# Kernel tuning notes

Measured on AMD Instinct MI355X. Metric: run time of the kernel, lower is better.

The kernel has to match this reference:

```python
import jax, jax.numpy as jnp
import numpy as np

N, E, IN, HID, H, OUT = 50000, 1600000, 64, 128, 4, 64
D = HID // H  # per-head dim = 32
EPS = 1e-5
NEG_SLOPE = 0.2


def layer_norm(x, g, b):
    mu = x.mean(-1, keepdims=True)
    var = ((x - mu) ** 2).mean(-1, keepdims=True)
    return (x - mu) * jax.lax.rsqrt(var + EPS) * g + b


def gat_conv(h, src, dst, W, a_src, a_dst, bias):
    # h: [N, HID]; W: [HID, H*D]; a_src/a_dst: [H, D]
    hW = (h @ W).reshape(N, H, D)
    e_src = (hW * a_src).sum(-1)  # [N, H]
    e_dst = (hW * a_dst).sum(-1)  # [N, H]
    e = jax.nn.leaky_relu(e_src[src] + e_dst[dst], NEG_SLOPE)  # [Etot, H]
    m = jax.ops.segment_max(e, dst, num_segments=N)            # [N, H]
    ex = jnp.exp(e - m[dst])
    denom = jax.ops.segment_sum(ex, dst, num_segments=N)       # [N, H]
    alpha = ex / denom[dst]                                    # [Etot, H]
    out = jax.ops.segment_sum(alpha[:, :, None] * hW[src], dst, num_segments=N)
    return out.reshape(N, H * D) + bias


def setup_inputs():
    key = jax.random.key(0)
    ks = jax.random.split(key, 16)
    s = 0.05
    return {
        "x": jax.random.normal(ks[0], (N, IN), jnp.float32),
        "edge_index": jax.random.randint(ks[1], (2, E), 0, N, jnp.int64),
        "w_in": jax.random.normal(ks[2], (IN, HID), jnp.float32) * s,
        "b_in": jnp.zeros((HID,), jnp.float32),
        "g1": jnp.ones((HID,), jnp.float32),
        "be1": jnp.zeros((HID,), jnp.float32),
        "W1": jax.random.normal(ks[3], (HID, H * D), jnp.float32) * s,
        "as1": jax.random.normal(ks[4], (H, D), jnp.float32) * s,
        "ad1": jax.random.normal(ks[5], (H, D), jnp.float32) * s,
        "bg1": jnp.zeros((H * D,), jnp.float32),
        "g2": jnp.ones((HID,), jnp.float32),
        "be2": jnp.zeros((HID,), jnp.float32),
        "W2": jax.random.normal(ks[6], (HID, H * D), jnp.float32) * s,
        "as2": jax.random.normal(ks[7], (H, D), jnp.float32) * s,
        "ad2": jax.random.normal(ks[8], (H, D), jnp.float32) * s,
        "bg2": jnp.zeros((H * D,), jnp.float32),
        "w_out": jax.random.normal(ks[9], (HID, OUT), jnp.float32) * s,
        "b_out": jnp.zeros((OUT,), jnp.float32),
    }


def reference(x, edge_index, w_in, b_in, g1, be1, W1, as1, ad1, bg1,
              g2, be2, W2, as2, ad2, bg2, w_out, b_out):
    # PyG GATConv default add_self_loops=True
    loops = jnp.arange(N, dtype=edge_index.dtype)
    src = jnp.concatenate([edge_index[0], loops])
    dst = jnp.concatenate([edge_index[1], loops])

    h = x @ w_in + b_in
    h = jax.nn.gelu(layer_norm(h, g1, be1))
    h = gat_conv(h, src, dst, W1, as1, ad1, bg1)
    h = jax.nn.gelu(layer_norm(h, g2, be2))
    # dropout: identity in eval mode
    h = gat_conv(h, src, dst, W2, as2, ad2, bg2)
    return h @ w_out + b_out
```

## Files before the change

### kernel.cpp

```cpp
#include <hip/hip_runtime.h>
#include <hip/hip_bf16.h>
#include <math.h>

#define NN   50000
#define EE   1600000
#define ETOT (EE + NN)
#define HID  128
#define INF_ 64
#define OUTF 64

#define NBK  1024
#define NPB  49
#define CAP  3072
#define BBLK 256
#define CHUNK ((ETOT + BBLK - 1) / BBLK)

#define PADX 72
#define PADH 136

typedef short  short8  __attribute__((ext_vector_type(8)));
typedef float  floatx4 __attribute__((ext_vector_type(4)));
typedef float  floatx2 __attribute__((ext_vector_type(2)));

__device__ __forceinline__ ushort f2b(float f) {
    __hip_bfloat16 h = __float2bfloat16(f);
    return *reinterpret_cast<ushort*>(&h);
}

__device__ __forceinline__ float gelu_f(float x) {
    float x2 = x * x;
    float u  = 0.7978845608f * fmaf(0.044715f * x2, x, x);
    u = fminf(u, 40.f);
    float t = __expf(2.f * u);
    return x * t / (t + 1.f);
}


__global__ __launch_bounds__(1024) void k_bucket(const int* __restrict__ ei,
                                                 int* bcur, int* __restrict__ tmp) {
    __shared__ unsigned sortedv[CHUNK];
    __shared__ int hist[NBK], gbase[NBK], loff[NBK], lcur[NBK];
    int t = threadIdx.x;
    int lo = blockIdx.x * CHUNK;
    int hi = min(lo + CHUNK, ETOT);
    int bsize = hi - lo;
    hist[t] = 0;
    __syncthreads();
    for (int i = lo + t; i < hi; i += 1024) {
        int d = (i < EE) ? ei[EE + i] : i - EE;
        atomicAdd(&hist[d / NPB], 1);
    }
    __syncthreads();
    {
        int c = hist[t];
        gbase[t] = (c > 0) ? atomicAdd(&bcur[t], c) : 0;
        loff[t] = c;
    }
    __syncthreads();
    for (int d = 1; d < NBK; d <<= 1) {
        int v = (t >= d) ? loff[t - d] : 0;
        __syncthreads();
        loff[t] += v;
        __syncthreads();
    }
    {
        int ex = loff[t] - hist[t];
        __syncthreads();
        loff[t] = ex;
        lcur[t] = ex;
    }
    __syncthreads();
    for (int i = lo + t; i < hi; i += 1024) {
        unsigned s, d;
        if (i < EE) { s = (unsigned)ei[i]; d = (unsigned)ei[EE + i]; }
        else        { s = d = (unsigned)(i - EE); }
        unsigned b = d / NPB;
        int p = atomicAdd(&lcur[b], 1);
        sortedv[p] = (b << 22) | (s << 6) | (d - b * NPB);
    }
    __syncthreads();
    for (int i = t; i < bsize; i += 1024) {
        unsigned v = sortedv[i];
        unsigned b = v >> 22;
        int pp = gbase[b] + i - loff[b];
        if (pp < CAP) tmp[b * CAP + pp] = (int)(v & 0x3FFFFFu);
    }
}

__global__ __launch_bounds__(1024) void k_bscan(const int* __restrict__ bcur,
                                                int* __restrict__ bstart,
                                                int* __restrict__ off,
                                                int* __restrict__ csr) {
    __shared__ int s[NBK];
    int t = threadIdx.x;
    int v0 = bcur[t];
    s[t] = v0;
    __syncthreads();
    for (int d = 1; d < NBK; d <<= 1) {
        int v = (t >= d) ? s[t - d] : 0;
        __syncthreads();
        s[t] += v;
        __syncthreads();
    }
    bstart[t] = s[t] - v0;
    if (t == 0) off[NN] = ETOT;
    if (t < 64) csr[ETOT + t] = 0;
}

__global__ __launch_bounds__(256) void k_bucket2csr(const int* __restrict__ tmp,
                                                    const int* __restrict__ bcur,
                                                    const int* __restrict__ bstart,
                                                    int* __restrict__ off,
                                                    int* __restrict__ csr,
                                                    int* __restrict__ dstid) {
    __shared__ int sE[CAP];
    __shared__ int lcnt[NPB];
    __shared__ int loff[NPB];
    int b = blockIdx.x, t = threadIdx.x;
    int n0    = b * NPB;
    int bsize = min(bcur[b], CAP);
    int base  = bstart[b];
    if (t < NPB) lcnt[t] = 0;
    for (int i = t; i < bsize; i += 256) sE[i] = tmp[b * CAP + i];
    __syncthreads();
    for (int i = t; i < bsize; i += 256) atomicAdd(&lcnt[sE[i] & 63], 1);
    __syncthreads();
    if (t == 0) {
        int run = 0;
        for (int j = 0; j < NPB; ++j) { loff[j] = run; run += lcnt[j]; }
    }
    __syncthreads();
    if (t < NPB) {
        if (n0 + t < NN) off[n0 + t] = base + loff[t];
        lcnt[t] = loff[t];
    }
    __syncthreads();
    for (int i = t; i < bsize; i += 256) {
        int v   = sE[i];
        int d   = v & 63;
        int pos = base + atomicAdd(&lcnt[d], 1);
        csr[pos]   = v >> 6;
        dstid[pos] = n0 + d;
    }
}


__global__ void k_packall(const float* __restrict__ w_in, const float* __restrict__ W1,
                          const float* __restrict__ W2, ushort* __restrict__ Bp1,
                          ushort* __restrict__ BpW1, ushort* __restrict__ BpW2,
                          int* __restrict__ bcur) {
    int tid = blockIdx.x * 256 + threadIdx.x;
    if (tid < NBK) bcur[tid] = 0;
    const float* W; ushort* dst; int K, id;
    if (tid < 1024)      { W = w_in; dst = Bp1;  K = 64;  id = tid; }
    else if (tid < 3072) { W = W1;   dst = BpW1; K = 128; id = tid - 1024; }
    else if (tid < 5120) { W = W2;   dst = BpW2; K = 128; id = tid - 3072; }
    else return;
    int kst = K >> 5;
    int l = id & 63;
    int s = (id >> 6) % kst;
    int T = id / (kst * 64);
    int m = l & 15, q = l >> 4;
    ushort o[8];
    #pragma unroll
    for (int j = 0; j < 8; ++j)
        o[j] = f2b(W[(s * 32 + q * 8 + j) * 128 + T * 16 + m]);
    uint4 pk;
    pk.x = (unsigned)o[0] | ((unsigned)o[1] << 16);
    pk.y = (unsigned)o[2] | ((unsigned)o[3] << 16);
    pk.z = (unsigned)o[4] | ((unsigned)o[5] << 16);
    pk.w = (unsigned)o[6] | ((unsigned)o[7] << 16);
    reinterpret_cast<uint4*>(dst)[id] = pk;
}

__device__ __forceinline__ void pack_store_fp8(ushort* hbfw, int l, int n0w, bool active,
                                               uint* __restrict__ hW8) {
    if (!active) return;
    int row = l >> 2, ch = l & 3;
    uint ov[8];
    #pragma unroll
    for (int u = 0; u < 8; ++u) {
        int c0 = ch * 32 + u * 4;
        float f0 = __uint_as_float((uint)hbfw[row * PADH + c0 + 0] << 16);
        float f1 = __uint_as_float((uint)hbfw[row * PADH + c0 + 1] << 16);
        float f2 = __uint_as_float((uint)hbfw[row * PADH + c0 + 2] << 16);
        float f3 = __uint_as_float((uint)hbfw[row * PADH + c0 + 3] << 16);
        int pk = __builtin_amdgcn_cvt_pk_fp8_f32(f0, f1, 0, false);
        pk     = __builtin_amdgcn_cvt_pk_fp8_f32(f2, f3, pk, true);
        ov[u] = (uint)pk;
    }
    uint4* dst = reinterpret_cast<uint4*>(hW8 + (size_t)(n0w + row) * 32 + ch * 8);
    dst[0] = make_uint4(ov[0], ov[1], ov[2], ov[3]);
    dst[1] = make_uint4(ov[4], ov[5], ov[6], ov[7]);
}


__global__ __launch_bounds__(128) void k_infeat(const float* __restrict__ x,
                                                const ushort* __restrict__ Bp1,
                                                const float* __restrict__ bin,
                                                const float* __restrict__ g,
                                                const float* __restrict__ be,
                                                const ushort* __restrict__ Bp2,
                                                const float* __restrict__ asrc,
                                                const float* __restrict__ adst,
                                                uint* __restrict__ hW8,
                                                float* __restrict__ esrc,
                                                float* __restrict__ edst) {
    __shared__ ushort xbf[2][16 * PADX];
    __shared__ ushort hbf[2][16 * PADH];
    int t = threadIdx.x, w = t >> 6, l = t & 63;
    int m = l & 15, q = l >> 4;
    int n0w = blockIdx.x * 32 + w * 16;
    bool active = (n0w < NN);
    int nb = active ? n0w : 0;

    const float4* x4 = reinterpret_cast<const float4*>(x) + (size_t)nb * 16;
    #pragma unroll
    for (int i = 0; i < 4; ++i) {
        int f4 = l + 64 * i;
        int node = f4 >> 4, c4 = f4 & 15;
        float4 v = x4[f4];
        ushort4 pk = { f2b(v.x), f2b(v.y), f2b(v.z), f2b(v.w) };
        *reinterpret_cast<ushort4*>(&xbf[w][node * PADX + c4 * 4]) = pk;
    }
    __syncthreads();

    const short8* B1 = reinterpret_cast<const short8*>(Bp1);
    floatx4 acc1[8];
    #pragma unroll
    for (int T = 0; T < 8; ++T) acc1[T] = (floatx4){0.f, 0.f, 0.f, 0.f};
    #pragma unroll
    for (int s = 0; s < 2; ++s) {
        short8 a = *reinterpret_cast<const short8*>(&xbf[w][m * PADX + s * 32 + q * 8]);
        #pragma unroll
        for (int T = 0; T < 8; ++T) {
            short8 b = B1[(T * 2 + s) * 64 + l];
            acc1[T] = __builtin_amdgcn_mfma_f32_16x16x32_bf16(a, b, acc1[T], 0, 0, 0);
        }
    }

    float bc[8], gc[8], bec[8];
    #pragma unroll
    for (int T = 0; T < 8; ++T) {
        int c = T * 16 + m;
        bc[T] = bin[c]; gc[T] = g[c]; bec[T] = be[c];
    }
    #pragma unroll
    for (int j = 0; j < 4; ++j) {
        float s1 = 0.f, s2 = 0.f;
        #pragma unroll
        for (int T = 0; T < 8; ++T) {
            float v = acc1[T][j] + bc[T];
            s1 += v; s2 = fmaf(v, v, s2);
        }
        #pragma unroll
        for (int mk = 1; mk < 16; mk <<= 1) {
            s1 += __shfl_xor(s1, mk, 64);
            s2 += __shfl_xor(s2, mk, 64);
        }
        float mu = s1 * (1.f / 128.f);
        float var = s2 * (1.f / 128.f) - mu * mu;
        float rs = rsqrtf(var + 1e-5f);
        #pragma unroll
        for (int T = 0; T < 8; ++T) {
            float v = acc1[T][j] + bc[T];
            float y = (v - mu) * rs * gc[T] + bec[T];
            hbf[w][(q * 4 + j) * PADH + T * 16 + m] = f2b(gelu_f(y));
        }
    }
    __syncthreads();

    const short8* B2 = reinterpret_cast<const short8*>(Bp2);
    floatx4 acc2[8];
    #pragma unroll
    for (int T = 0; T < 8; ++T) acc2[T] = (floatx4){0.f, 0.f, 0.f, 0.f};
    #pragma unroll
    for (int s = 0; s < 4; ++s) {
        short8 a = *reinterpret_cast<const short8*>(&hbf[w][m * PADH + s * 32 + q * 8]);
        #pragma unroll
        for (int T = 0; T < 8; ++T) {
            short8 b = B2[(T * 4 + s) * 64 + l];
            acc2[T] = __builtin_amdgcn_mfma_f32_16x16x32_bf16(a, b, acc2[T], 0, 0, 0);
        }
    }

    __syncthreads();
    #pragma unroll
    for (int j = 0; j < 4; ++j)
        #pragma unroll
        for (int T = 0; T < 8; ++T)
            hbf[w][(q * 4 + j) * PADH + T * 16 + m] = f2b(acc2[T][j]);
    __syncthreads();
    pack_store_fp8(hbf[w], l, n0w, active, hW8);

    float as_[8], ad_[8];
    #pragma unroll
    for (int T = 0; T < 8; ++T) {
        int c = T * 16 + m;
        as_[T] = asrc[c]; ad_[T] = adst[c];
    }
    #pragma unroll
    for (int j = 0; j < 4; ++j) {
        #pragma unroll
        for (int h = 0; h < 4; ++h) {
            float v1 = fmaf(acc2[2 * h][j], as_[2 * h], acc2[2 * h + 1][j] * as_[2 * h + 1]);
            float v2 = fmaf(acc2[2 * h][j], ad_[2 * h], acc2[2 * h + 1][j] * ad_[2 * h + 1]);
            #pragma unroll
            for (int mk = 1; mk < 16; mk <<= 1) {
                v1 += __shfl_xor(v1, mk, 64);
                v2 += __shfl_xor(v2, mk, 64);
            }
            if (m == 0 && active) {
                esrc[(n0w + q * 4 + j) * 4 + h] = v1;
                edst[(n0w + q * 4 + j) * 4 + h] = v2;
            }
        }
    }
}


__global__ __launch_bounds__(128) void k_feat(const float* __restrict__ hin,
                                              const float* __restrict__ g,
                                              const float* __restrict__ be,
                                              const ushort* __restrict__ Bp2,
                                              const float* __restrict__ asrc,
                                              const float* __restrict__ adst,
                                              uint* __restrict__ hW8,
                                              float* __restrict__ esrc,
                                              float* __restrict__ edst) {
    __shared__ ushort hbf[2][16 * PADH];
    int t = threadIdx.x, w = t >> 6, l = t & 63;
    int m = l & 15, q = l >> 4;
    int n0w = blockIdx.x * 32 + w * 16;
    bool active = (n0w < NN);
    int nb = active ? n0w : 0;

    const float4* h4g = reinterpret_cast<const float4*>(hin) + (size_t)nb * 32;
    const float4* g4  = reinterpret_cast<const float4*>(g);
    const float4* be4 = reinterpret_cast<const float4*>(be);
    #pragma unroll
    for (int i = 0; i < 8; ++i) {
        int f4 = l + 64 * i;
        int node = f4 >> 5, c4 = f4 & 31;
        float4 v = h4g[f4];
        float s1 = v.x + v.y + v.z + v.w;
        float s2 = fmaf(v.x, v.x, fmaf(v.y, v.y, fmaf(v.z, v.z, v.w * v.w)));
        #pragma unroll
        for (int mk = 1; mk < 32; mk <<= 1) {
            s1 += __shfl_xor(s1, mk, 64);
            s2 += __shfl_xor(s2, mk, 64);
        }
        float mu = s1 * (1.f / 128.f);
        float var = s2 * (1.f / 128.f) - mu * mu;
        float rs = rsqrtf(var + 1e-5f);
        float4 gg = g4[c4], bb = be4[c4];
        ushort4 pk;
        pk.x = f2b(gelu_f((v.x - mu) * rs * gg.x + bb.x));
        pk.y = f2b(gelu_f((v.y - mu) * rs * gg.y + bb.y));
        pk.z = f2b(gelu_f((v.z - mu) * rs * gg.z + bb.z));
        pk.w = f2b(gelu_f((v.w - mu) * rs * gg.w + bb.w));
        *reinterpret_cast<ushort4*>(&hbf[w][node * PADH + c4 * 4]) = pk;
    }
    __syncthreads();

    const short8* B2 = reinterpret_cast<const short8*>(Bp2);
    floatx4 acc2[8];
    #pragma unroll
    for (int T = 0; T < 8; ++T) acc2[T] = (floatx4){0.f, 0.f, 0.f, 0.f};
    #pragma unroll
    for (int s = 0; s < 4; ++s) {
        short8 a = *reinterpret_cast<const short8*>(&hbf[w][m * PADH + s * 32 + q * 8]);
        #pragma unroll
        for (int T = 0; T < 8; ++T) {
            short8 b = B2[(T * 4 + s) * 64 + l];
            acc2[T] = __builtin_amdgcn_mfma_f32_16x16x32_bf16(a, b, acc2[T], 0, 0, 0);
        }
    }

    __syncthreads();
    #pragma unroll
    for (int j = 0; j < 4; ++j)
        #pragma unroll
        for (int T = 0; T < 8; ++T)
            hbf[w][(q * 4 + j) * PADH + T * 16 + m] = f2b(acc2[T][j]);
    __syncthreads();
    pack_store_fp8(hbf[w], l, n0w, active, hW8);

    float as_[8], ad_[8];
    #pragma unroll
    for (int T = 0; T < 8; ++T) {
        int c = T * 16 + m;
        as_[T] = asrc[c]; ad_[T] = adst[c];
    }
    #pragma unroll
    for (int j = 0; j < 4; ++j) {
        #pragma unroll
        for (int h = 0; h < 4; ++h) {
            float v1 = fmaf(acc2[2 * h][j], as_[2 * h], acc2[2 * h + 1][j] * as_[2 * h + 1]);
            float v2 = fmaf(acc2[2 * h][j], ad_[2 * h], acc2[2 * h + 1][j] * ad_[2 * h + 1]);
            #pragma unroll
            for (int mk = 1; mk < 16; mk <<= 1) {
                v1 += __shfl_xor(v1, mk, 64);
                v2 += __shfl_xor(v2, mk, 64);
            }
            if (m == 0 && active) {
                esrc[(n0w + q * 4 + j) * 4 + h] = v1;
                edst[(n0w + q * 4 + j) * 4 + h] = v2;
            }
        }
    }
}


__global__ __launch_bounds__(256) void k_edgew(const int* __restrict__ csr,
                                               const int* __restrict__ dstid,
                                               const float* __restrict__ esrc,
                                               const float* __restrict__ edst,
                                               ushort* __restrict__ wexp) {
    int i = blockIdx.x * 256 + threadIdx.x;
    if (i >= ETOT) return;
    int s = csr[i], d = dstid[i];
    float4 es = reinterpret_cast<const float4*>(esrc)[s];
    float4 ed = reinterpret_cast<const float4*>(edst)[d];
    float e0 = es.x + ed.x, e1 = es.y + ed.y, e2 = es.z + ed.z, e3 = es.w + ed.w;
    e0 = __expf(fmaxf(e0, 0.2f * e0));
    e1 = __expf(fmaxf(e1, 0.2f * e1));
    e2 = __expf(fmaxf(e2, 0.2f * e2));
    e3 = __expf(fmaxf(e3, 0.2f * e3));
    ushort4 pk = { f2b(e0), f2b(e1), f2b(e2), f2b(e3) };
    reinterpret_cast<ushort4*>(wexp)[i] = pk;
}


__global__ __launch_bounds__(128) void k_gat(const uint* __restrict__ hW8,
                                             const ushort* __restrict__ wexp,
                                             const int* __restrict__ off,
                                             const int* __restrict__ csr,
                                             const float* __restrict__ bg,
                                             float* __restrict__ out) {
    __shared__ float redA[16][8];
    __shared__ float redD[16];
    int n = blockIdx.x, t = threadIdx.x;
    int wv = t >> 6, l = t & 63;
    int slot = l >> 4;
    int q    = l & 15;
    int hq   = q >> 2;
    int o0 = off[n], o1 = off[n + 1];
    const uint2* hw2 = reinterpret_cast<const uint2*>(hW8);
    floatx2 a01 = {0.f, 0.f}, a23 = {0.f, 0.f}, a45 = {0.f, 0.f}, a67 = {0.f, 0.f};
    float dsum = 0.f;
    int nIter = (o1 - o0 + 15) >> 4;
    int e = o0 + wv * 4 + slot;

    int    srcA = csr[e];      ushort ubA = wexp[e * 4 + hq];
    int    srcB = csr[e + 8];  ushort ubB = wexp[(e + 8) * 4 + hq];
    int    srcC = csr[e + 16]; ushort ubC = wexp[(e + 16) * 4 + hq];
    int    srcD = csr[e + 24]; ushort ubD = wexp[(e + 24) * 4 + hq];
    uint2  rA = hw2[(size_t)srcA * 16 + q];
    uint2  rB = hw2[(size_t)srcB * 16 + q];

    for (int it = 0; it < nIter; ++it) {
        uint2 rC = hw2[(size_t)srcC * 16 + q];
        uint2 rD = hw2[(size_t)srcD * 16 + q];
        int    srcE = csr[e + 32]; ushort ubE = wexp[(e + 32) * 4 + hq];
        int    srcF = csr[e + 40]; ushort ubF = wexp[(e + 40) * 4 + hq];
        float wa = (e     < o1) ? __uint_as_float(((unsigned)ubA) << 16) : 0.f;
        float wb = (e + 8 < o1) ? __uint_as_float(((unsigned)ubB) << 16) : 0.f;
        floatx2 wa2 = {wa, wa}, wb2 = {wb, wb};
        a01 += wa2 * __builtin_amdgcn_cvt_pk_f32_fp8(rA.x, false);
        a23 += wa2 * __builtin_amdgcn_cvt_pk_f32_fp8(rA.x, true);
        a45 += wa2 * __builtin_amdgcn_cvt_pk_f32_fp8(rA.y, false);
        a67 += wa2 * __builtin_amdgcn_cvt_pk_f32_fp8(rA.y, true);
        a01 += wb2 * __builtin_amdgcn_cvt_pk_f32_fp8(rB.x, false);
        a23 += wb2 * __builtin_amdgcn_cvt_pk_f32_fp8(rB.x, true);
        a45 += wb2 * __builtin_amdgcn_cvt_pk_f32_fp8(rB.y, false);
        a67 += wb2 * __builtin_amdgcn_cvt_pk_f32_fp8(rB.y, true);
        dsum += wa + wb;
        e += 16;
        rA = rC; rB = rD;
        srcC = srcE; srcD = srcF;
        ubA = ubC; ubB = ubD; ubC = ubE; ubD = ubF;
    }
    float acc[8] = {a01[0], a01[1], a23[0], a23[1], a45[0], a45[1], a67[0], a67[1]};
    #pragma unroll
    for (int mk = 16; mk <= 32; mk <<= 1) {
        #pragma unroll
        for (int j = 0; j < 8; ++j) acc[j] += __shfl_xor(acc[j], mk, 64);
        dsum += __shfl_xor(dsum, mk, 64);
    }
    if (wv == 1 && l < 16) {
        #pragma unroll
        for (int j = 0; j < 8; ++j) redA[l][j] = acc[j];
        redD[l] = dsum;
    }
    __syncthreads();
    if (wv == 0 && l < 16) {
        float inv = 1.0f / (dsum + redD[l]);
        float4 r0, r1;
        r0.x = (acc[0] + redA[l][0]) * inv + bg[l * 8 + 0];
        r0.y = (acc[1] + redA[l][1]) * inv + bg[l * 8 + 1];
        r0.z = (acc[2] + redA[l][2]) * inv + bg[l * 8 + 2];
        r0.w = (acc[3] + redA[l][3]) * inv + bg[l * 8 + 3];
        r1.x = (acc[4] + redA[l][4]) * inv + bg[l * 8 + 4];
        r1.y = (acc[5] + redA[l][5]) * inv + bg[l * 8 + 5];
        r1.z = (acc[6] + redA[l][6]) * inv + bg[l * 8 + 6];
        r1.w = (acc[7] + redA[l][7]) * inv + bg[l * 8 + 7];
        float4* op = reinterpret_cast<float4*>(out + (size_t)n * HID + l * 8);
        op[0] = r0; op[1] = r1;
    }
}


__global__ __launch_bounds__(64) void k_out(const float* __restrict__ h,
                                            const float* __restrict__ w,
                                            const float* __restrict__ b,
                                            float* __restrict__ out) {
    __shared__ __align__(16) float hr[16 * 132];
    int t = threadIdx.x, n0 = blockIdx.x * 16;
    const float4* h4g = reinterpret_cast<const float4*>(h) + (size_t)n0 * 32;
    float4* hr4 = reinterpret_cast<float4*>(hr);
    #pragma unroll
    for (int i = 0; i < 8; ++i) {
        int f4 = t + 64 * i;
        hr4[(f4 >> 5) * 33 + (f4 & 31)] = h4g[f4];
    }
    __syncthreads();
    int cg = t & 15, ng = t >> 4;
    const float4* w4 = reinterpret_cast<const float4*>(w);
    float4 bb = reinterpret_cast<const float4*>(b)[cg];
    float4 acc[4] = {bb, bb, bb, bb};
    for (int k4 = 0; k4 < 32; ++k4) {
        float4 w0 = w4[(k4 * 4 + 0) * 16 + cg];
        float4 w1 = w4[(k4 * 4 + 1) * 16 + cg];
        float4 w2 = w4[(k4 * 4 + 2) * 16 + cg];
        float4 w3 = w4[(k4 * 4 + 3) * 16 + cg];
        #pragma unroll
        for (int r = 0; r < 4; ++r) {
            float4 hv = hr4[(ng * 4 + r) * 33 + k4];
            acc[r].x = fmaf(hv.x, w0.x, fmaf(hv.y, w1.x, fmaf(hv.z, w2.x, fmaf(hv.w, w3.x, acc[r].x))));
            acc[r].y = fmaf(hv.x, w0.y, fmaf(hv.y, w1.y, fmaf(hv.z, w2.y, fmaf(hv.w, w3.y, acc[r].y))));
            acc[r].z = fmaf(hv.x, w0.z, fmaf(hv.y, w1.z, fmaf(hv.z, w2.z, fmaf(hv.w, w3.z, acc[r].z))));
            acc[r].w = fmaf(hv.x, w0.w, fmaf(hv.y, w1.w, fmaf(hv.z, w2.w, fmaf(hv.w, w3.w, acc[r].w))));
        }
    }
    float4* o4 = reinterpret_cast<float4*>(out) + (size_t)n0 * 16;
    #pragma unroll
    for (int r = 0; r < 4; ++r) o4[(ng * 4 + r) * 16 + cg] = acc[r];
}

extern "C" void kernel_launch(void* const* d_in, const int* in_sizes, int n_in,
                              void* d_out, int out_size, void* d_ws, size_t ws_size,
                              hipStream_t stream) {
    const float* x    = (const float*)d_in[0];
    const int*   ei   = (const int*)  d_in[1];
    const float* w_in = (const float*)d_in[2];
    const float* b_in = (const float*)d_in[3];
    const float* g1   = (const float*)d_in[4];
    const float* be1  = (const float*)d_in[5];
    const float* W1   = (const float*)d_in[6];
    const float* as1  = (const float*)d_in[7];
    const float* ad1  = (const float*)d_in[8];
    const float* bg1  = (const float*)d_in[9];
    const float* g2   = (const float*)d_in[10];
    const float* be2  = (const float*)d_in[11];
    const float* W2   = (const float*)d_in[12];
    const float* as2  = (const float*)d_in[13];
    const float* ad2  = (const float*)d_in[14];
    const float* bg2  = (const float*)d_in[15];
    const float* w_o  = (const float*)d_in[16];
    const float* b_o  = (const float*)d_in[17];
    float* out = (float*)d_out;

    char* p = (char*)d_ws;
    auto take = [&](size_t bytes) {
        void* r = p;
        p += (bytes + 255) & ~(size_t)255;
        return r;
    };
    float*  gout  = (float*)take((size_t)NN * HID * 4);
    float*  h2    = (float*)take((size_t)NN * HID * 4);
    uint*   hW8   = (uint*)take((size_t)NN * HID);
    float*  esrc  = (float*)take((size_t)NN * 4 * 4);
    float*  edst  = (float*)take((size_t)NN * 4 * 4);
    int*    off   = (int*)take((size_t)(NN + 1) * 4);
    int*    csr   = (int*)take((size_t)(ETOT + 64) * 4);
    int*    dstid = (int*)take((size_t)ETOT * 4);
    size_t ovl = (size_t)ETOT * 8 + 512;
    size_t tsz = (size_t)NBK * CAP * 4;
    ushort* wexp  = (ushort*)take(ovl > tsz ? ovl : tsz);
    int*    tmp   = (int*)wexp;
    int*    bcur  = (int*)take((size_t)NBK * 4);
    int*    bstart= (int*)take((size_t)NBK * 4);
    ushort* Bp1   = (ushort*)take((size_t)1024 * 16);
    ushort* BpW1  = (ushort*)take((size_t)2048 * 16);
    ushort* BpW2  = (ushort*)take((size_t)2048 * 16);

    k_packall   <<<20, 256, 0, stream>>>(w_in, W1, W2, Bp1, BpW1, BpW2, bcur);
    k_bucket    <<<BBLK, 1024, 0, stream>>>(ei, bcur, tmp);
    k_bscan     <<<1, NBK, 0, stream>>>(bcur, bstart, off, csr);
    k_bucket2csr<<<NBK, 256, 0, stream>>>(tmp, bcur, bstart, off, csr, dstid);

    int gfeat = (NN + 31) / 32;
    k_infeat<<<gfeat, 128, 0, stream>>>(x, Bp1, b_in, g1, be1, BpW1, as1, ad1, hW8, esrc, edst);
    k_edgew <<<(ETOT + 255) / 256, 256, 0, stream>>>(csr, dstid, esrc, edst, wexp);
    k_gat   <<<NN, 128, 0, stream>>>(hW8, wexp, off, csr, bg1, gout);
    k_feat  <<<gfeat, 128, 0, stream>>>(gout, g2, be2, BpW2, as2, ad2, hW8, esrc, edst);
    k_edgew <<<(ETOT + 255) / 256, 256, 0, stream>>>(csr, dstid, esrc, edst, wexp);
    k_gat   <<<NN, 128, 0, stream>>>(hW8, wexp, off, csr, bg2, h2);
    k_out   <<<NN / 16, 64, 0, stream>>>(h2, w_o, b_o, out);
}
```

Baseline: 304.4 us.

## Fuse edge attention weights into GAT aggregation and drop dstid/wexp buffers

Removes the separate k_edgew pass, so the aggregation kernel now computes the leaky-relu and exp of esrc[src]+edst[dst] inline from per-node scores. This eliminates the dstid array and the bf16 wexp buffer along with their global writes and reads. The CSR build now uses 256 buckets of 196 nodes with a larger capacity, and k_bucket2csr uses 512 threads and a parallel scan. k_out processes 32 nodes per block with a bounds guard. The trade-off is a dependent gather of esrc per edge plus an exp per edge inside k_gat, and a larger per-bucket shared memory footprint in the CSR build.

```diff
diff --git a/kernel.cpp b/kernel.cpp
--- a/kernel.cpp
+++ b/kernel.cpp
@@ -9,9 +9,9 @@
 #define INF_ 64
 #define OUTF 64
 
-#define NBK  1024
-#define NPB  49
-#define CAP  3072
+#define NBK  256
+#define NPB  196
+#define CAP  8192
 #define BBLK 256
 #define CHUNK ((ETOT + BBLK - 1) / BBLK)
 
@@ -44,28 +44,27 @@
     int lo = blockIdx.x * CHUNK;
     int hi = min(lo + CHUNK, ETOT);
     int bsize = hi - lo;
-    hist[t] = 0;
+    if (t < NBK) hist[t] = 0;
     __syncthreads();
     for (int i = lo + t; i < hi; i += 1024) {
         int d = (i < EE) ? ei[EE + i] : i - EE;
         atomicAdd(&hist[d / NPB], 1);
     }
     __syncthreads();
-    {
+    if (t < NBK) {
         int c = hist[t];
         gbase[t] = (c > 0) ? atomicAdd(&bcur[t], c) : 0;
         loff[t] = c;
     }
     __syncthreads();
     for (int d = 1; d < NBK; d <<= 1) {
-        int v = (t >= d) ? loff[t - d] : 0;
+        int v = (t >= d && t < NBK) ? loff[t - d] : 0;
         __syncthreads();
-        loff[t] += v;
+        if (t < NBK) loff[t] += v;
         __syncthreads();
     }
-    {
+    if (t < NBK) {
         int ex = loff[t] - hist[t];
-        __syncthreads();
         loff[t] = ex;
         lcur[t] = ex;
     }
@@ -76,21 +75,21 @@
         else        { s = d = (unsigned)(i - EE); }
         unsigned b = d / NPB;
         int p = atomicAdd(&lcur[b], 1);
-        sortedv[p] = (b << 22) | (s << 6) | (d - b * NPB);
+        sortedv[p] = (b << 24) | (s << 8) | (d - b * NPB);
     }
     __syncthreads();
     for (int i = t; i < bsize; i += 1024) {
         unsigned v = sortedv[i];
-        unsigned b = v >> 22;
+        unsigned b = v >> 24;
         int pp = gbase[b] + i - loff[b];
-        if (pp < CAP) tmp[b * CAP + pp] = (int)(v & 0x3FFFFFu);
-    }
-}
-
-__global__ __launch_bounds__(1024) void k_bscan(const int* __restrict__ bcur,
-                                                int* __restrict__ bstart,
-                                                int* __restrict__ off,
-                                                int* __restrict__ csr) {
+        if (pp < CAP) tmp[b * CAP + pp] = (int)(v & 0xFFFFFFu);
+    }
+}
+
+__global__ __launch_bounds__(256) void k_bscan(const int* __restrict__ bcur,
+                                               int* __restrict__ bstart,
+                                               int* __restrict__ off,
+                                               int* __restrict__ csr) {
     __shared__ int s[NBK];
     int t = threadIdx.x;
     int v0 = bcur[t];
@@ -107,12 +106,11 @@
     if (t < 64) csr[ETOT + t] = 0;
 }
 
-__global__ __launch_bounds__(256) void k_bucket2csr(const int* __restrict__ tmp,
+__global__ __launch_bounds__(512) void k_bucket2csr(const int* __restrict__ tmp,
                                                     const int* __restrict__ bcur,
                                                     const int* __restrict__ bstart,
                                                     int* __restrict__ off,
-                                                    int* __restrict__ csr,
-                                                    int* __restrict__ dstid) {
+                                                    int* __restrict__ csr) {
     __shared__ int sE[CAP];
     __shared__ int lcnt[NPB];
     __shared__ int loff[NPB];
@@ -121,26 +119,28 @@
     int bsize = min(bcur[b], CAP);
     int base  = bstart[b];
     if (t < NPB) lcnt[t] = 0;
-    for (int i = t; i < bsize; i += 256) sE[i] = tmp[b * CAP + i];
-    __syncthreads();
-    for (int i = t; i < bsize; i += 256) atomicAdd(&lcnt[sE[i] & 63], 1);
-    __syncthreads();
-    if (t == 0) {
-        int run = 0;
-        for (int j = 0; j < NPB; ++j) { loff[j] = run; run += lcnt[j]; }
-    }
-    __syncthreads();
+    for (int i = t; i < bsize; i += 512) sE[i] = tmp[b * CAP + i];
+    __syncthreads();
+    for (int i = t; i < bsize; i += 512) atomicAdd(&lcnt[sE[i] & 255], 1);
+    __syncthreads();
+    if (t < NPB) loff[t] = lcnt[t];
+    __syncthreads();
+    for (int d = 1; d < NPB; d <<= 1) {
+        int v = (t >= d && t < NPB) ? loff[t - d] : 0;
+        __syncthreads();
+        if (t < NPB) loff[t] += v;
+        __syncthreads();
+    }
     if (t < NPB) {
-        if (n0 + t < NN) off[n0 + t] = base + loff[t];
-        lcnt[t] = loff[t];
-    }
-    __syncthreads();
-    for (int i = t; i < bsize; i += 256) {
+        int ex = loff[t] - lcnt[t];
+        if (n0 + t < NN) off[n0 + t] = base + ex;
+        lcnt[t] = ex;
+    }
+    __syncthreads();
+    for (int i = t; i < bsize; i += 512) {
         int v   = sE[i];
-        int d   = v & 63;
-        int pos = base + atomicAdd(&lcnt[d], 1);
-        csr[pos]   = v >> 6;
-        dstid[pos] = n0 + d;
+        int pos = base + atomicAdd(&lcnt[v & 255], 1);
+        csr[pos] = v >> 8;
     }
 }
 
@@ -172,6 +172,7 @@
     pk.w = (unsigned)o[6] | ((unsigned)o[7] << 16);
     reinterpret_cast<uint4*>(dst)[id] = pk;
 }
+
 
 __device__ __forceinline__ void pack_store_fp8(ushort* hbfw, int l, int n0w, bool active,
                                                uint* __restrict__ hW8) {
@@ -412,28 +413,9 @@
 }
 
 
-__global__ __launch_bounds__(256) void k_edgew(const int* __restrict__ csr,
-                                               const int* __restrict__ dstid,
-                                               const float* __restrict__ esrc,
-                                               const float* __restrict__ edst,
-                                               ushort* __restrict__ wexp) {
-    int i = blockIdx.x * 256 + threadIdx.x;
-    if (i >= ETOT) return;
-    int s = csr[i], d = dstid[i];
-    float4 es = reinterpret_cast<const float4*>(esrc)[s];
-    float4 ed = reinterpret_cast<const float4*>(edst)[d];
-    float e0 = es.x + ed.x, e1 = es.y + ed.y, e2 = es.z + ed.z, e3 = es.w + ed.w;
-    e0 = __expf(fmaxf(e0, 0.2f * e0));
-    e1 = __expf(fmaxf(e1, 0.2f * e1));
-    e2 = __expf(fmaxf(e2, 0.2f * e2));
-    e3 = __expf(fmaxf(e3, 0.2f * e3));
-    ushort4 pk = { f2b(e0), f2b(e1), f2b(e2), f2b(e3) };
-    reinterpret_cast<ushort4*>(wexp)[i] = pk;
-}
-
-
 __global__ __launch_bounds__(128) void k_gat(const uint* __restrict__ hW8,
-                                             const ushort* __restrict__ wexp,
+                                             const float* __restrict__ esrc,
+                                             const float* __restrict__ edst,
                                              const int* __restrict__ off,
                                              const int* __restrict__ csr,
                                              const float* __restrict__ bg,
@@ -446,26 +428,33 @@
     int q    = l & 15;
     int hq   = q >> 2;
     int o0 = off[n], o1 = off[n + 1];
+    float ednh = edst[n * 4 + hq];
     const uint2* hw2 = reinterpret_cast<const uint2*>(hW8);
     floatx2 a01 = {0.f, 0.f}, a23 = {0.f, 0.f}, a45 = {0.f, 0.f}, a67 = {0.f, 0.f};
     float dsum = 0.f;
     int nIter = (o1 - o0 + 15) >> 4;
     int e = o0 + wv * 4 + slot;
 
-    int    srcA = csr[e];      ushort ubA = wexp[e * 4 + hq];
-    int    srcB = csr[e + 8];  ushort ubB = wexp[(e + 8) * 4 + hq];
-    int    srcC = csr[e + 16]; ushort ubC = wexp[(e + 16) * 4 + hq];
-    int    srcD = csr[e + 24]; ushort ubD = wexp[(e + 24) * 4 + hq];
-    uint2  rA = hw2[(size_t)srcA * 16 + q];
-    uint2  rB = hw2[(size_t)srcB * 16 + q];
+    int srcA = csr[e];
+    int srcB = csr[e + 8];
+    int srcC = csr[e + 16];
+    int srcD = csr[e + 24];
+    float esA = esrc[srcA * 4 + hq];
+    float esB = esrc[srcB * 4 + hq];
+    uint2 rA = hw2[(size_t)srcA * 16 + q];
+    uint2 rB = hw2[(size_t)srcB * 16 + q];
 
     for (int it = 0; it < nIter; ++it) {
         uint2 rC = hw2[(size_t)srcC * 16 + q];
         uint2 rD = hw2[(size_t)srcD * 16 + q];
-        int    srcE = csr[e + 32]; ushort ubE = wexp[(e + 32) * 4 + hq];
-        int    srcF = csr[e + 40]; ushort ubF = wexp[(e + 40) * 4 + hq];
-        float wa = (e     < o1) ? __uint_as_float(((unsigned)ubA) << 16) : 0.f;
-        float wb = (e + 8 < o1) ? __uint_as_float(((unsigned)ubB) << 16) : 0.f;
+        float esC = esrc[srcC * 4 + hq];
+        float esD = esrc[srcD * 4 + hq];
+        int srcE = csr[e + 32];
+        int srcF = csr[e + 40];
+        float ea = esA + ednh; ea = fmaxf(ea, 0.2f * ea);
+        float eb = esB + ednh; eb = fmaxf(eb, 0.2f * eb);
+        float wa = (e     < o1) ? __expf(ea) : 0.f;
+        float wb = (e + 8 < o1) ? __expf(eb) : 0.f;
         floatx2 wa2 = {wa, wa}, wb2 = {wb, wb};
         a01 += wa2 * __builtin_amdgcn_cvt_pk_f32_fp8(rA.x, false);
         a23 += wa2 * __builtin_amdgcn_cvt_pk_f32_fp8(rA.x, true);
@@ -478,8 +467,8 @@
         dsum += wa + wb;
         e += 16;
         rA = rC; rB = rD;
+        esA = esC; esB = esD;
         srcC = srcE; srcD = srcF;
-        ubA = ubC; ubB = ubD; ubC = ubE; ubD = ubF;
     }
     float acc[8] = {a01[0], a01[1], a23[0], a23[1], a45[0], a45[1], a67[0], a67[1]};
     #pragma unroll
@@ -511,17 +500,17 @@
 }
 
 
-__global__ __launch_bounds__(64) void k_out(const float* __restrict__ h,
-                                            const float* __restrict__ w,
-                                            const float* __restrict__ b,
-                                            float* __restrict__ out) {
-    __shared__ __align__(16) float hr[16 * 132];
-    int t = threadIdx.x, n0 = blockIdx.x * 16;
+__global__ __launch_bounds__(128) void k_out(const float* __restrict__ h,
+                                             const float* __restrict__ w,
+                                             const float* __restrict__ b,
+                                             float* __restrict__ out) {
+    __shared__ __align__(16) float hr[32 * 132];
+    int t = threadIdx.x, n0 = blockIdx.x * 32;
     const float4* h4g = reinterpret_cast<const float4*>(h) + (size_t)n0 * 32;
     float4* hr4 = reinterpret_cast<float4*>(hr);
     #pragma unroll
     for (int i = 0; i < 8; ++i) {
-        int f4 = t + 64 * i;
+        int f4 = t + 128 * i;
         hr4[(f4 >> 5) * 33 + (f4 & 31)] = h4g[f4];
     }
     __syncthreads();
@@ -545,7 +534,10 @@
     }
     float4* o4 = reinterpret_cast<float4*>(out) + (size_t)n0 * 16;
     #pragma unroll
-    for (int r = 0; r < 4; ++r) o4[(ng * 4 + r) * 16 + cg] = acc[r];
+    for (int r = 0; r < 4; ++r) {
+        if (n0 + ng * 4 + r < NN)
+            o4[(ng * 4 + r) * 16 + cg] = acc[r];
+    }
 }
 
 extern "C" void kernel_launch(void* const* d_in, const int* in_sizes, int n_in,
@@ -584,11 +576,7 @@
     float*  edst  = (float*)take((size_t)NN * 4 * 4);
     int*    off   = (int*)take((size_t)(NN + 1) * 4);
     int*    csr   = (int*)take((size_t)(ETOT + 64) * 4);
-    int*    dstid = (int*)take((size_t)ETOT * 4);
-    size_t ovl = (size_t)ETOT * 8 + 512;
-    size_t tsz = (size_t)NBK * CAP * 4;
-    ushort* wexp  = (ushort*)take(ovl > tsz ? ovl : tsz);
-    int*    tmp   = (int*)wexp;
+    int*    tmp   = (int*)take((size_t)NBK * CAP * 4);
     int*    bcur  = (int*)take((size_t)NBK * 4);
     int*    bstart= (int*)take((size_t)NBK * 4);
     ushort* Bp1   = (ushort*)take((size_t)1024 * 16);
@@ -598,14 +586,12 @@
     k_packall   <<<20, 256, 0, stream>>>(w_in, W1, W2, Bp1, BpW1, BpW2, bcur);
     k_bucket    <<<BBLK, 1024, 0, stream>>>(ei, bcur, tmp);
     k_bscan     <<<1, NBK, 0, stream>>>(bcur, bstart, off, csr);
-    k_bucket2csr<<<NBK, 256, 0, stream>>>(tmp, bcur, bstart, off, csr, dstid);
+    k_bucket2csr<<<NBK, 512, 0, stream>>>(tmp, bcur, bstart, off, csr);
 
     int gfeat = (NN + 31) / 32;
     k_infeat<<<gfeat, 128, 0, stream>>>(x, Bp1, b_in, g1, be1, BpW1, as1, ad1, hW8, esrc, edst);
-    k_edgew <<<(ETOT + 255) / 256, 256, 0, stream>>>(csr, dstid, esrc, edst, wexp);
-    k_gat   <<<NN, 128, 0, stream>>>(hW8, wexp, off, csr, bg1, gout);
+    k_gat   <<<NN, 128, 0, stream>>>(hW8, esrc, edst, off, csr, bg1, gout);
     k_feat  <<<gfeat, 128, 0, stream>>>(gout, g2, be2, BpW2, as2, ad2, hW8, esrc, edst);
-    k_edgew <<<(ETOT + 255) / 256, 256, 0, stream>>>(csr, dstid, esrc, edst, wexp);
-    k_gat   <<<NN, 128, 0, stream>>>(hW8, wexp, off, csr, bg2, h2);
-    k_out   <<<NN / 16, 64, 0, stream>>>(h2, w_o, b_o, out);
-}
+    k_gat   <<<NN, 128, 0, stream>>>(hW8, esrc, edst, off, csr, bg2, h2);
+    k_out   <<<(NN + 31) / 32, 128, 0, stream>>>(h2, w_o, b_o, out);
+}
```

After: 282.4 us. 7.2% less time.
